# Optimization experiments

Hardware: AMD Instinct MI355X
Metric: run time of the kernel (lower is better)

The kernel has to match this reference:

```python
import jax, jax.numpy as jnp
import numpy as np

B, L, D, K, V = 128, 50, 64, 1024, 100000


def setup_inputs() -> dict:
    key = jax.random.key(0)
    ks = jax.random.split(key, 10)
    s = 0.05
    return {
        "history_item_ids": jax.random.randint(ks[0], (B, L), 0, V, dtype=jnp.int32),
        "history_item_masks": jax.random.randint(ks[1], (B, L), 0, 2, dtype=jnp.int32),
        "embedding_table": jax.random.normal(ks[2], (V, D), jnp.float32) * s,
        "code_book": jax.random.normal(ks[3], (K, D), jnp.float32) * 0.1,
        "Wq": jax.random.normal(ks[4], (D, D), jnp.float32) * s,
        "bq": jnp.zeros((D,), jnp.float32),
        "Wk": jax.random.normal(ks[5], (D, D), jnp.float32) * s,
        "bk": jnp.zeros((D,), jnp.float32),
        "Wv": jax.random.normal(ks[6], (D, D), jnp.float32) * s,
        "bv": jnp.zeros((D,), jnp.float32),
        "W_enc": jax.random.normal(ks[7], (2 * D, D), jnp.float32) * s,
        "b_enc": jnp.zeros((D,), jnp.float32),
    }


def reference(history_item_ids, history_item_masks, embedding_table, code_book,
              Wq, bq, Wk, bk, Wv, bv, W_enc, b_enc):
    # mask out padded history positions
    mask = (history_item_masks >= 1).astype(jnp.float32)          # [B, L]
    h = embedding_table[history_item_ids] * mask[..., None]       # [B, L, D]

    # self_attn: attention over ALL B*L flattened tokens (cross-batch, as original)
    flat = h.reshape(-1, D)                                       # [B*L, D]
    q = flat @ Wq + bq
    k = flat @ Wk + bk
    v = flat @ Wv + bv
    scores = (q @ k.T) / jnp.sqrt(jnp.float32(D))                 # [B*L, B*L]
    h = (jax.nn.softmax(scores, axis=-1) @ v).reshape(B, L, D)

    denom = mask.sum(axis=1, keepdims=True)                       # [B, 1]
    hist_mean = h.sum(axis=1) / (denom + 1e-9)                    # [B, D]

    # get_quantized: pairwise sq distances + argmin + codebook lookup
    f = h.reshape(-1, D)                                          # [B*L, D]
    d2 = (jnp.sum(f * f, axis=1, keepdims=True)
          + jnp.sum(code_book * code_book, axis=1)
          - 2.0 * f @ code_book.T)                                # [B*L, K]
    idx = jnp.argmin(d2, axis=1)                                  # [B*L]
    vq = code_book[idx].reshape(B, L, D)                          # one_hot @ code_book == gather
    vq_mean = vq.sum(axis=1) / denom                              # [B, D]

    x = jnp.concatenate([vq_mean, hist_mean], axis=-1)            # [B, 2D]
    return x @ W_enc + b_enc                                      # [B, D]
```

## Files before the change

### kernel.cpp

```cpp
#include <hip/hip_runtime.h>

typedef __attribute__((ext_vector_type(8))) short bf16x8_t;
typedef __attribute__((ext_vector_type(4))) float f32x4_t;

#define B_   128
#define L_   50
#define D_   64
#define N_   6400
#define KC   1024
#define STRD 72

static __device__ __forceinline__ unsigned short f2b(float x) {
    union { float f; unsigned int u; } c; c.f = x;
    return (unsigned short)((c.u + 0x7FFFu + ((c.u >> 16) & 1u)) >> 16);
}

__global__ __launch_bounds__(256) void k_qkv(
    const int* __restrict__ ids, const int* __restrict__ masks,
    const float* __restrict__ emb,
    const float* __restrict__ Wq, const float* __restrict__ bq,
    const float* __restrict__ Wk, const float* __restrict__ bk,
    const float* __restrict__ Wv, const float* __restrict__ bv,
    const float* __restrict__ cbf,
    unsigned short* __restrict__ q, unsigned short* __restrict__ k,
    unsigned short* __restrict__ vt,
    float* __restrict__ cn, unsigned short* __restrict__ cbb)
{
    const int tid = threadIdx.x;
    if (blockIdx.x >= 400) {
        const int c = (blockIdx.x - 400) * 256 + tid;
        float s = 0.f;
        #pragma unroll
        for (int d4 = 0; d4 < 16; ++d4) {
            float4 x = ((const float4*)cbf)[c * 16 + d4];
            s = fmaf(x.x, x.x, s); s = fmaf(x.y, x.y, s);
            s = fmaf(x.z, x.z, s); s = fmaf(x.w, x.w, s);
            ushort4 u;
            u.x = f2b(x.x); u.y = f2b(x.y); u.z = f2b(x.z); u.w = f2b(x.w);
            *(ushort4*)&cbb[c * 64 + d4 * 4] = u;
        }
        cn[c] = s;
        return;
    }

    __shared__ float Ws[3 * 64 * 64];
    __shared__ float hs[16][64];
    const int n0  = blockIdx.x * 16;

    {
        const float4* wq4 = (const float4*)Wq;
        const float4* wk4 = (const float4*)Wk;
        const float4* wv4 = (const float4*)Wv;
        float4* ws4 = (float4*)Ws;
        #pragma unroll
        for (int i = 0; i < 4; ++i) ws4[i*256 + tid]        = wq4[i*256 + tid];
        #pragma unroll
        for (int i = 0; i < 4; ++i) ws4[1024 + i*256 + tid] = wk4[i*256 + tid];
        #pragma unroll
        for (int i = 0; i < 4; ++i) ws4[2048 + i*256 + tid] = wv4[i*256 + tid];
    }
    {
        const int t  = tid >> 4, c4 = tid & 15;
        const int n  = n0 + t;
        const int id = ids[n];
        const float m = (masks[n] >= 1) ? 1.0f : 0.0f;
        float4 e = ((const float4*)emb)[id * 16 + c4];
        ((float4*)&hs[t][0])[c4] = make_float4(e.x*m, e.y*m, e.z*m, e.w*m);
    }
    __syncthreads();

    const int j  = tid & 63;
    const int tg = tid >> 6;
    const float bqj = bq[j], bkj = bk[j], bvj = bv[j];
    #pragma unroll
    for (int p = 0; p < 4; ++p) {
        const int t = p * 4 + tg;
        float aq = bqj, ak = bkj, av = bvj;
        #pragma unroll 8
        for (int d = 0; d < 64; ++d) {
            const float hd = hs[t][d];
            aq = fmaf(hd, Ws[d*64 + j],        aq);
            ak = fmaf(hd, Ws[4096 + d*64 + j], ak);
            av = fmaf(hd, Ws[8192 + d*64 + j], av);
        }
        const int n = n0 + t;
        q[n*64 + j]   = f2b(aq);
        k[n*64 + j]   = f2b(ak);
        vt[j*N_ + n]  = f2b(av);
    }
}

__global__ __launch_bounds__(256, 2) void k_attn(
    const unsigned short* __restrict__ qg, const unsigned short* __restrict__ kg,
    const unsigned short* __restrict__ vtg,
    float* __restrict__ facc, float* __restrict__ lacc)
{
    __shared__ unsigned short Qs[32 * STRD];
    __shared__ unsigned short Ks[64 * STRD];
    __shared__ unsigned short Vts[64 * STRD];
    __shared__ unsigned short Ps[32 * STRD];
    __shared__ float Of[32 * 66];
    __shared__ float lred[2][32];

    const int tid  = threadIdx.x;
    const int qt   = blockIdx.x >> 2;
    const int sp   = blockIdx.x & 3;
    const int q0   = qt * 32;
    const int kvb  = sp * 1600;
    const int lane = tid & 63;
    const int w    = tid >> 6;
    const int m    = w & 1;
    const int s    = w >> 1;
    const int lr   = lane & 15;
    const int lg   = lane >> 4;

    {
        const int row = tid >> 3, ch = tid & 7;
        uint4 t = *(const uint4*)&qg[(q0 + row) * 64 + ch * 8];
        *(uint4*)&Qs[row * STRD + ch * 8] = t;
    }
    __syncthreads();
    const bf16x8_t qa0 = *(const bf16x8_t*)&Qs[(m*16 + lr) * STRD +  0 + lg*8];
    const bf16x8_t qa1 = *(const bf16x8_t*)&Qs[(m*16 + lr) * STRD + 32 + lg*8];

    f32x4_t o0 = {0.f,0.f,0.f,0.f}, o1 = {0.f,0.f,0.f,0.f};
    f32x4_t o2 = {0.f,0.f,0.f,0.f}, o3 = {0.f,0.f,0.f,0.f};
    float ls0 = 0.f, ls1 = 0.f, ls2 = 0.f, ls3 = 0.f;
    const float scale = 0.125f;

    for (int st = 0; st < 25; ++st) {
        __syncthreads();
        const int j0 = kvb + st * 64;
        {
            const int row = tid >> 3, ch = tid & 7;
            uint4 a = *(const uint4*)&kg [(j0 + row)      * 64 + ch*8];
            uint4 b = *(const uint4*)&kg [(j0 + row + 32) * 64 + ch*8];
            uint4 c = *(const uint4*)&vtg[ row       * N_ + j0 + ch*8];
            uint4 d = *(const uint4*)&vtg[(row + 32) * N_ + j0 + ch*8];
            *(uint4*)&Ks [ row      * STRD + ch*8] = a;
            *(uint4*)&Ks [(row+32)  * STRD + ch*8] = b;
            *(uint4*)&Vts[ row      * STRD + ch*8] = c;
            *(uint4*)&Vts[(row+32)  * STRD + ch*8] = d;
        }
        __syncthreads();

        #pragma unroll
        for (int t = 0; t < 2; ++t) {
            const int kcol = s*32 + t*16 + lr;
            bf16x8_t kb0 = *(const bf16x8_t*)&Ks[kcol * STRD +  0 + lg*8];
            bf16x8_t kb1 = *(const bf16x8_t*)&Ks[kcol * STRD + 32 + lg*8];
            f32x4_t acc = {0.f,0.f,0.f,0.f};
            acc = __builtin_amdgcn_mfma_f32_16x16x32_bf16(qa0, kb0, acc, 0, 0, 0);
            acc = __builtin_amdgcn_mfma_f32_16x16x32_bf16(qa1, kb1, acc, 0, 0, 0);
            const float p0 = __expf(acc[0] * scale);
            const float p1 = __expf(acc[1] * scale);
            const float p2 = __expf(acc[2] * scale);
            const float p3 = __expf(acc[3] * scale);
            ls0 += p0; ls1 += p1; ls2 += p2; ls3 += p3;
            const int rb = (m*16 + lg*4) * STRD + kcol;
            Ps[rb           ] = f2b(p0);
            Ps[rb +   STRD  ] = f2b(p1);
            Ps[rb + 2*STRD  ] = f2b(p2);
            Ps[rb + 3*STRD  ] = f2b(p3);
        }

        const bf16x8_t pa = *(const bf16x8_t*)&Ps[(m*16 + lr) * STRD + s*32 + lg*8];
        {
            bf16x8_t vb;
            vb = *(const bf16x8_t*)&Vts[( 0 + lr) * STRD + s*32 + lg*8];
            o0 = __builtin_amdgcn_mfma_f32_16x16x32_bf16(pa, vb, o0, 0, 0, 0);
            vb = *(const bf16x8_t*)&Vts[(16 + lr) * STRD + s*32 + lg*8];
            o1 = __builtin_amdgcn_mfma_f32_16x16x32_bf16(pa, vb, o1, 0, 0, 0);
            vb = *(const bf16x8_t*)&Vts[(32 + lr) * STRD + s*32 + lg*8];
            o2 = __builtin_amdgcn_mfma_f32_16x16x32_bf16(pa, vb, o2, 0, 0, 0);
            vb = *(const bf16x8_t*)&Vts[(48 + lr) * STRD + s*32 + lg*8];
            o3 = __builtin_amdgcn_mfma_f32_16x16x32_bf16(pa, vb, o3, 0, 0, 0);
        }
    }

    #pragma unroll
    for (int off = 1; off <= 8; off <<= 1) {
        ls0 += __shfl_xor(ls0, off);
        ls1 += __shfl_xor(ls1, off);
        ls2 += __shfl_xor(ls2, off);
        ls3 += __shfl_xor(ls3, off);
    }
    if (lr == 0) {
        const int rb = m*16 + lg*4;
        lred[s][rb    ] = ls0;
        lred[s][rb + 1] = ls1;
        lred[s][rb + 2] = ls2;
        lred[s][rb + 3] = ls3;
    }

    if (s == 0) {
        #pragma unroll
        for (int r = 0; r < 4; ++r) {
            const int row = m*16 + lg*4 + r;
            Of[row*66 +  0 + lr] = o0[r];
            Of[row*66 + 16 + lr] = o1[r];
            Of[row*66 + 32 + lr] = o2[r];
            Of[row*66 + 48 + lr] = o3[r];
        }
    }
    __syncthreads();
    if (s == 1) {
        #pragma unroll
        for (int r = 0; r < 4; ++r) {
            const int row = m*16 + lg*4 + r;
            float* dst = &facc[(q0 + row) * 64];
            atomicAdd(&dst[ 0 + lr], Of[row*66 +  0 + lr] + o0[r]);
            atomicAdd(&dst[16 + lr], Of[row*66 + 16 + lr] + o1[r]);
            atomicAdd(&dst[32 + lr], Of[row*66 + 32 + lr] + o2[r]);
            atomicAdd(&dst[48 + lr], Of[row*66 + 48 + lr] + o3[r]);
        }
    }
    if (tid < 32) atomicAdd(&lacc[q0 + tid], lred[0][tid] + lred[1][tid]);
}

__global__ __launch_bounds__(64) void k_argmin(
    const float* __restrict__ facc, const float* __restrict__ lacc,
    const unsigned short* __restrict__ cbb,
    const float* __restrict__ cn, int* __restrict__ idx)
{
    const int lane = threadIdx.x;
    const int n0   = blockIdx.x * 16;
    const int lr   = lane & 15, lg = lane >> 4;
    const int row  = n0 + lr;

    const float inv = 1.0f / lacc[row];
    float4 a0 = *(const float4*)&facc[row*64 +      lg*8];
    float4 a1 = *(const float4*)&facc[row*64 +      lg*8 + 4];
    float4 a2 = *(const float4*)&facc[row*64 + 32 + lg*8];
    float4 a3 = *(const float4*)&facc[row*64 + 32 + lg*8 + 4];
    bf16x8_t fa0, fa1;
    fa0[0] = (short)f2b(a0.x*inv); fa0[1] = (short)f2b(a0.y*inv);
    fa0[2] = (short)f2b(a0.z*inv); fa0[3] = (short)f2b(a0.w*inv);
    fa0[4] = (short)f2b(a1.x*inv); fa0[5] = (short)f2b(a1.y*inv);
    fa0[6] = (short)f2b(a1.z*inv); fa0[7] = (short)f2b(a1.w*inv);
    fa1[0] = (short)f2b(a2.x*inv); fa1[1] = (short)f2b(a2.y*inv);
    fa1[2] = (short)f2b(a2.z*inv); fa1[3] = (short)f2b(a2.w*inv);
    fa1[4] = (short)f2b(a3.x*inv); fa1[5] = (short)f2b(a3.y*inv);
    fa1[6] = (short)f2b(a3.z*inv); fa1[7] = (short)f2b(a3.w*inv);

    float best0 = 3.0e38f, best1 = 3.0e38f, best2 = 3.0e38f, best3 = 3.0e38f;
    int   bi0 = 0, bi1 = 0, bi2 = 0, bi3 = 0;

    #pragma unroll 4
    for (int st = 0; st < 64; ++st) {
        const int crow = st * 16 + lr;
        bf16x8_t cb0 = *(const bf16x8_t*)&cbb[crow * 64 +  0 + lg*8];
        bf16x8_t cb1 = *(const bf16x8_t*)&cbb[crow * 64 + 32 + lg*8];
        const float cnv = cn[crow];
        f32x4_t acc = {0.f,0.f,0.f,0.f};
        acc = __builtin_amdgcn_mfma_f32_16x16x32_bf16(fa0, cb0, acc, 0, 0, 0);
        acc = __builtin_amdgcn_mfma_f32_16x16x32_bf16(fa1, cb1, acc, 0, 0, 0);
        const float d0 = fmaf(-2.f, acc[0], cnv);
        const float d1 = fmaf(-2.f, acc[1], cnv);
        const float d2 = fmaf(-2.f, acc[2], cnv);
        const float d3 = fmaf(-2.f, acc[3], cnv);
        if (d0 < best0) { best0 = d0; bi0 = crow; }
        if (d1 < best1) { best1 = d1; bi1 = crow; }
        if (d2 < best2) { best2 = d2; bi2 = crow; }
        if (d3 < best3) { best3 = d3; bi3 = crow; }
    }

    #pragma unroll
    for (int off = 1; off <= 8; off <<= 1) {
        float ov; int oi;
        ov = __shfl_xor(best0, off); oi = __shfl_xor(bi0, off);
        if (ov < best0 || (ov == best0 && oi < bi0)) { best0 = ov; bi0 = oi; }
        ov = __shfl_xor(best1, off); oi = __shfl_xor(bi1, off);
        if (ov < best1 || (ov == best1 && oi < bi1)) { best1 = ov; bi1 = oi; }
        ov = __shfl_xor(best2, off); oi = __shfl_xor(bi2, off);
        if (ov < best2 || (ov == best2 && oi < bi2)) { best2 = ov; bi2 = oi; }
        ov = __shfl_xor(best3, off); oi = __shfl_xor(bi3, off);
        if (ov < best3 || (ov == best3 && oi < bi3)) { best3 = ov; bi3 = oi; }
    }
    if (lr == 0) {
        idx[n0 + lg*4 + 0] = bi0;
        idx[n0 + lg*4 + 1] = bi1;
        idx[n0 + lg*4 + 2] = bi2;
        idx[n0 + lg*4 + 3] = bi3;
    }
}

__global__ __launch_bounds__(64) void k_final(
    const float* __restrict__ facc, const float* __restrict__ lacc,
    const float* __restrict__ cb,
    const int* __restrict__ idx, const int* __restrict__ masks,
    const float* __restrict__ Wenc, const float* __restrict__ benc,
    float* __restrict__ out)
{
    __shared__ float xs[128];
    const int b = blockIdx.x, d = threadIdx.x;
    float vq = 0.f, hi = 0.f, dn = 0.f;
    for (int l = 0; l < L_; ++l) {
        const int n = b * L_ + l;
        vq += cb[idx[n]*64 + d];
        hi += facc[n*64 + d] * (1.0f / lacc[n]);
        dn += (masks[n] >= 1) ? 1.0f : 0.0f;
    }
    xs[d]      = vq / dn;
    xs[64 + d] = hi / (dn + 1e-9f);
    __syncthreads();
    float acc = benc[d];
    #pragma unroll 8
    for (int t = 0; t < 128; ++t) acc = fmaf(xs[t], Wenc[t*64 + d], acc);
    out[b*64 + d] = acc;
}

extern "C" void kernel_launch(void* const* d_in, const int* in_sizes, int n_in,
                              void* d_out, int out_size, void* d_ws, size_t ws_size,
                              hipStream_t stream)
{
    const int*   ids   = (const int*)  d_in[0];
    const int*   masks = (const int*)  d_in[1];
    const float* emb   = (const float*)d_in[2];
    const float* cb    = (const float*)d_in[3];
    const float* Wq    = (const float*)d_in[4];
    const float* bq    = (const float*)d_in[5];
    const float* Wk    = (const float*)d_in[6];
    const float* bk    = (const float*)d_in[7];
    const float* Wv    = (const float*)d_in[8];
    const float* bv    = (const float*)d_in[9];
    const float* Wenc  = (const float*)d_in[10];
    const float* benc  = (const float*)d_in[11];
    float* out = (float*)d_out;

    char* w = (char*)d_ws;
    unsigned short* qb   = (unsigned short*)(w);
    unsigned short* kb   = (unsigned short*)(w +  819200);
    unsigned short* vtb  = (unsigned short*)(w + 1638400);
    float*          facc = (float*)        (w + 2457600);
    float*          lacc = (float*)        (w + 4096000);
    float*          cn   = (float*)        (w + 4121600);
    unsigned short* cbb  = (unsigned short*)(w + 4125696);
    int*            idxp = (int*)          (w + 4256768);

    hipMemsetAsync(w + 2457600, 0, 1638400 + 25600, stream);

    hipLaunchKernelGGL(k_qkv,    dim3(404), dim3(256), 0, stream,
                       ids, masks, emb, Wq, bq, Wk, bk, Wv, bv, cb,
                       qb, kb, vtb, cn, cbb);
    hipLaunchKernelGGL(k_attn,   dim3(800), dim3(256), 0, stream,
                       qb, kb, vtb, facc, lacc);
    hipLaunchKernelGGL(k_argmin, dim3(400), dim3(64),  0, stream,
                       facc, lacc, cbb, cn, idxp);
    hipLaunchKernelGGL(k_final,  dim3(128), dim3(64),  0, stream,
                       facc, lacc, cb, idxp, masks, Wenc, benc, out);
}
```

Baseline: 177.9 us.

## Fuse zeroing into qkv kernel, move per-batch reductions into argmin

After: 172.7 us. 2.9% less time.

```diff
diff --git a/kernel.cpp b/kernel.cpp
--- a/kernel.cpp
+++ b/kernel.cpp
@@ -24,9 +24,16 @@
     const float* __restrict__ cbf,
     unsigned short* __restrict__ q, unsigned short* __restrict__ k,
     unsigned short* __restrict__ vt,
-    float* __restrict__ cn, unsigned short* __restrict__ cbb)
+    float* __restrict__ cn, unsigned short* __restrict__ cbb,
+    float4* __restrict__ zbase)
 {
     const int tid = threadIdx.x;
+    if (blockIdx.x >= 404) {
+        const float4 z = make_float4(0.f, 0.f, 0.f, 0.f);
+        for (int i = (blockIdx.x - 404) * 256 + tid; i < 108096; i += 26 * 256)
+            zbase[i] = z;
+        return;
+    }
     if (blockIdx.x >= 400) {
         const int c = (blockIdx.x - 400) * 256 + tid;
         float s = 0.f;
@@ -90,7 +97,7 @@
     }
 }
 
-__global__ __launch_bounds__(256, 2) void k_attn(
+__global__ __launch_bounds__(256, 4) void k_attn(
     const unsigned short* __restrict__ qg, const unsigned short* __restrict__ kg,
     const unsigned short* __restrict__ vtg,
     float* __restrict__ facc, float* __restrict__ lacc)
@@ -221,14 +228,18 @@
 __global__ __launch_bounds__(64) void k_argmin(
     const float* __restrict__ facc, const float* __restrict__ lacc,
     const unsigned short* __restrict__ cbb,
-    const float* __restrict__ cn, int* __restrict__ idx)
-{
+    const float* __restrict__ cn, const float* __restrict__ cbf,
+    float* __restrict__ vqsum, float* __restrict__ hisum)
+{
+    __shared__ int   sidx[16];
+    __shared__ float sinv[16];
     const int lane = threadIdx.x;
     const int n0   = blockIdx.x * 16;
     const int lr   = lane & 15, lg = lane >> 4;
     const int row  = n0 + lr;
 
     const float inv = 1.0f / lacc[row];
+    if (lg == 0) sinv[lr] = inv;
     float4 a0 = *(const float4*)&facc[row*64 +      lg*8];
     float4 a1 = *(const float4*)&facc[row*64 +      lg*8 + 4];
     float4 a2 = *(const float4*)&facc[row*64 + 32 + lg*8];
@@ -278,31 +289,44 @@
         if (ov < best3 || (ov == best3 && oi < bi3)) { best3 = ov; bi3 = oi; }
     }
     if (lr == 0) {
-        idx[n0 + lg*4 + 0] = bi0;
-        idx[n0 + lg*4 + 1] = bi1;
-        idx[n0 + lg*4 + 2] = bi2;
-        idx[n0 + lg*4 + 3] = bi3;
+        sidx[lg*4 + 0] = bi0;
+        sidx[lg*4 + 1] = bi1;
+        sidx[lg*4 + 2] = bi2;
+        sidx[lg*4 + 3] = bi3;
+    }
+    __syncthreads();
+
+    const int d  = lane;
+    const int b0 = n0 / 50;
+    const int r0 = n0 - b0 * 50;
+    float vq0 = 0.f, hi0 = 0.f, vq1 = 0.f, hi1 = 0.f;
+    #pragma unroll
+    for (int t = 0; t < 16; ++t) {
+        const float hv = facc[(n0 + t) * 64 + d] * sinv[t];
+        const float vv = cbf[sidx[t] * 64 + d];
+        if (r0 + t < 50) { vq0 += vv; hi0 += hv; }
+        else             { vq1 += vv; hi1 += hv; }
+    }
+    atomicAdd(&vqsum[b0*64 + d], vq0);
+    atomicAdd(&hisum[b0*64 + d], hi0);
+    if (r0 + 15 >= 50) {
+        atomicAdd(&vqsum[(b0+1)*64 + d], vq1);
+        atomicAdd(&hisum[(b0+1)*64 + d], hi1);
     }
 }
 
 __global__ __launch_bounds__(64) void k_final(
-    const float* __restrict__ facc, const float* __restrict__ lacc,
-    const float* __restrict__ cb,
-    const int* __restrict__ idx, const int* __restrict__ masks,
+    const float* __restrict__ vqsum, const float* __restrict__ hisum,
+    const int* __restrict__ masks,
     const float* __restrict__ Wenc, const float* __restrict__ benc,
     float* __restrict__ out)
 {
     __shared__ float xs[128];
     const int b = blockIdx.x, d = threadIdx.x;
-    float vq = 0.f, hi = 0.f, dn = 0.f;
-    for (int l = 0; l < L_; ++l) {
-        const int n = b * L_ + l;
-        vq += cb[idx[n]*64 + d];
-        hi += facc[n*64 + d] * (1.0f / lacc[n]);
-        dn += (masks[n] >= 1) ? 1.0f : 0.0f;
-    }
-    xs[d]      = vq / dn;
-    xs[64 + d] = hi / (dn + 1e-9f);
+    float dn = 0.f;
+    for (int l = 0; l < L_; ++l) dn += (masks[b*L_ + l] >= 1) ? 1.0f : 0.0f;
+    xs[d]      = vqsum[b*64 + d] / dn;
+    xs[64 + d] = hisum[b*64 + d] / (dn + 1e-9f);
     __syncthreads();
     float acc = benc[d];
     #pragma unroll 8
@@ -329,24 +353,24 @@
     float* out = (float*)d_out;
 
     char* w = (char*)d_ws;
-    unsigned short* qb   = (unsigned short*)(w);
-    unsigned short* kb   = (unsigned short*)(w +  819200);
-    unsigned short* vtb  = (unsigned short*)(w + 1638400);
-    float*          facc = (float*)        (w + 2457600);
-    float*          lacc = (float*)        (w + 4096000);
-    float*          cn   = (float*)        (w + 4121600);
-    unsigned short* cbb  = (unsigned short*)(w + 4125696);
-    int*            idxp = (int*)          (w + 4256768);
-
-    hipMemsetAsync(w + 2457600, 0, 1638400 + 25600, stream);
-
-    hipLaunchKernelGGL(k_qkv,    dim3(404), dim3(256), 0, stream,
+    unsigned short* qb    = (unsigned short*)(w);
+    unsigned short* kb    = (unsigned short*)(w +  819200);
+    unsigned short* vtb   = (unsigned short*)(w + 1638400);
+    float*          facc  = (float*)        (w + 2457600);
+    float*          lacc  = (float*)        (w + 4096000);
+    float*          vqsum = (float*)        (w + 4121600);
+    float*          hisum = (float*)        (w + 4154368);
+    float*          cn    = (float*)        (w + 4187136);
+    unsigned short* cbb   = (unsigned short*)(w + 4191232);
+    float4*         zbase = (float4*)       (w + 2457600);
+
+    hipLaunchKernelGGL(k_qkv,    dim3(430), dim3(256), 0, stream,
                        ids, masks, emb, Wq, bq, Wk, bk, Wv, bv, cb,
-                       qb, kb, vtb, cn, cbb);
+                       qb, kb, vtb, cn, cbb, zbase);
     hipLaunchKernelGGL(k_attn,   dim3(800), dim3(256), 0, stream,
                        qb, kb, vtb, facc, lacc);
     hipLaunchKernelGGL(k_argmin, dim3(400), dim3(64),  0, stream,
-                       facc, lacc, cbb, cn, idxp);
+                       facc, lacc, cbb, cn, cb, vqsum, hisum);
     hipLaunchKernelGGL(k_final,  dim3(128), dim3(64),  0, stream,
-                       facc, lacc, cb, idxp, masks, Wenc, benc, out);
-}
+                       vqsum, hisum, masks, Wenc, benc, out);
+}
```
